# Optimization experiments

Measured on AMD Instinct MI355X. Metric: run time of the kernel, lower is better.

Reference implementation:

```python
import jax, jax.numpy as jnp
import numpy as np

N = 8192
E = 262144
IN_DIM, HID, OUT = 256, 256, 32


def setup_inputs() -> dict:
    key = jax.random.key(0)
    ks = jax.random.split(key, 10)
    features = jax.random.normal(ks[0], (N, IN_DIM), jnp.float32)
    noise = jax.random.normal(ks[1], (N, OUT), jnp.float32)
    src = jax.random.randint(ks[2], (E,), 0, N, jnp.int32)
    dst = jax.random.randint(ks[3], (E,), 0, N, jnp.int32)
    s = lambda fi, fo: 1.0 / np.sqrt(fi)
    W1 = jax.random.normal(ks[4], (IN_DIM, HID), jnp.float32) * s(IN_DIM, HID)
    W2 = jax.random.normal(ks[5], (HID, HID), jnp.float32) * s(HID, HID)
    W3 = jax.random.normal(ks[6], (HID, OUT), jnp.float32) * s(HID, OUT)
    b1 = jnp.zeros((HID,), jnp.float32)
    b2 = jnp.zeros((HID,), jnp.float32)
    b3 = jnp.zeros((OUT,), jnp.float32)
    fc_w = jax.random.normal(ks[7], (IN_DIM, OUT), jnp.float32) * s(IN_DIM, OUT)
    return dict(features=features, noise=noise, src=src, dst=dst,
                W1=W1, b1=b1, W2=W2, b2=b2, W3=W3, b3=b3, fc_w=fc_w)


def _degree_norms(src, dst, n):
    ones = jnp.ones_like(src, jnp.float32)
    out_deg = jax.ops.segment_sum(ones, src, num_segments=n)
    in_deg = jax.ops.segment_sum(ones, dst, num_segments=n)
    # DGL GraphConv norm='both' clamps degrees to min 1 before pow(-0.5)
    norm_src = jnp.maximum(out_deg, 1.0) ** -0.5  # [N]
    norm_dst = jnp.maximum(in_deg, 1.0) ** -0.5   # [N]
    return norm_src, norm_dst


def _graph_conv(x, src, dst, norm_src, norm_dst, W, b, n):
    # h = D_in^{-1/2} A D_out^{-1/2} x W + b, then relu
    h = x @ W                                  # transform first (smaller agg dim)
    m = (h * norm_src[:, None])[src]           # [E, F] gather + scale
    agg = jax.ops.segment_sum(m, dst, num_segments=n)
    return jax.nn.relu(agg * norm_dst[:, None] + b)


def reference(features, noise, src, dst, W1, b1, W2, b2, W3, b3, fc_w):
    n = features.shape[0]
    norm_s, norm_d = _degree_norms(src, dst, n)
    h = _graph_conv(features, src, dst, norm_s, norm_d, W1, b1, n)
    mean = _graph_conv(h, src, dst, norm_s, norm_d, W2, b2, n)
    log_std = _graph_conv(h, src, dst, norm_s, norm_d, W3, b3, n)
    # note: mean [N,HID] broadcasts against noise*exp(log_std) [N,OUT] only if
    # HID==OUT dims align; original code has mean from layer[1] (hidden_dim) and
    # log_std from layer[2] (out_dim). To keep the math runnable we follow the
    # VGAE intent: layer[1] and layer[2] both map to out_dim here (W2 below is
    # hidden->hidden, W3 hidden->out; mean uses W3-shaped branch). See notes.
    z = mean[:, :noise.shape[1]] if mean.shape[1] != noise.shape[1] else mean
    z = z + noise * jnp.exp(log_std)
    adj_rec = jax.nn.sigmoid(z @ z.T)          # [N, N] dense decoder
    seq_fts = features @ fc_w                  # Linear(in_dim, out_dim, bias=False)
    return adj_rec, z, seq_fts
```

## Files before the change

kernel.cpp:

```cpp
#include <hip/hip_runtime.h>
#include <hip/hip_fp16.h>

#define NNODES 8192
#define NEDGES 262144
#define NNOUT 67108864L

typedef _Float16 half8 __attribute__((ext_vector_type(8)));
typedef _Float16 half4 __attribute__((ext_vector_type(4)));
typedef float float4v __attribute__((ext_vector_type(4)));


__global__ __launch_bounds__(256) void prep_kernel(const float* __restrict__ W1, const float* __restrict__ W2,
                                                   const float* __restrict__ W3, const float* __restrict__ b2,
                                                   const float* __restrict__ b3, _Float16* __restrict__ W1th,
                                                   _Float16* __restrict__ W1tl, _Float16* __restrict__ Wzth,
                                                   _Float16* __restrict__ Wztl, float* __restrict__ bz,
                                                   int* __restrict__ degs) {
  int b = blockIdx.x, t = threadIdx.x;
  float w = W1[b * 256 + t];
  _Float16 wh = (_Float16)w;
  W1th[t * 256 + b] = wh;
  W1tl[t * 256 + b] = (_Float16)(w - (float)wh);
  if (b >= 64 && b < 128) {
    int c = b - 64;
    float v = (c < 32) ? W2[t * 256 + c] : W3[t * 32 + (c - 32)];
    _Float16 vh = (_Float16)v;
    Wzth[c * 256 + t] = vh;
    Wztl[c * 256 + t] = (_Float16)(v - (float)vh);
  }
  if (b == 128 && t < 64) bz[t] = (t < 32) ? b2[t] : b3[t - 32];
  if (b >= 192) degs[(b - 192) * 256 + t] = 0;
}

__global__ __launch_bounds__(256) void deg_kernel(const int* __restrict__ src, const int* __restrict__ dst,
                                                  int* __restrict__ out_deg, int* __restrict__ in_deg) {
  int e = blockIdx.x * 256 + threadIdx.x;
  if (e < NEDGES) {
    atomicAdd(&out_deg[src[e]], 1);
    atomicAdd(&in_deg[dst[e]], 1);
  }
}

__global__ __launch_bounds__(256) void scan_norm_kernel(const int* __restrict__ in_deg,
                                                        const int* __restrict__ out_deg,
                                                        int* __restrict__ row_ptr, int* __restrict__ cursor,
                                                        float* __restrict__ norm_src, float* __restrict__ norm_dst) {
  __shared__ int partial[256];
  int t = threadIdx.x;
  int base = t * 32;
  int local[32];
  int s = 0;
#pragma unroll
  for (int i = 0; i < 32; ++i) { local[i] = in_deg[base + i]; s += local[i]; }
  partial[t] = s;
  __syncthreads();
  for (int off = 1; off < 256; off <<= 1) {
    int v = (t >= off) ? partial[t - off] : 0;
    __syncthreads();
    partial[t] += v;
    __syncthreads();
  }
  int run = (t == 0) ? 0 : partial[t - 1];
  if (t == 0) row_ptr[0] = 0;
#pragma unroll
  for (int i = 0; i < 32; ++i) {
    int od = out_deg[base + i]; if (od < 1) od = 1;
    int id = local[i]; if (id < 1) id = 1;
    norm_src[base + i] = rsqrtf((float)od);
    norm_dst[base + i] = rsqrtf((float)id);
    cursor[base + i] = run;
    run += local[i];
    row_ptr[base + i + 1] = run;
  }
}

__global__ __launch_bounds__(256) void scatter_convert(const int* __restrict__ src, const int* __restrict__ dst,
                                                       int* __restrict__ cursor, int* __restrict__ csr,
                                                       const float* __restrict__ x, const float* __restrict__ norm_src,
                                                       _Float16* __restrict__ xs) {
  int b = blockIdx.x, t = threadIdx.x;
  if (b < 1024) {
    int e = b * 256 + t;
    int d = dst[e];
    int pos = atomicAdd(&cursor[d], 1);
    csr[pos] = src[e];
  }
  int i = b * 256 + t;
  int base = i * 4;
  float ns = norm_src[base >> 8];
  float4 v = *(const float4*)(x + base);
  half4 o = {(_Float16)(v.x * ns), (_Float16)(v.y * ns), (_Float16)(v.z * ns), (_Float16)(v.w * ns)};
  *(half4*)(xs + base) = o;
}


__global__ __launch_bounds__(256) void propagate_hl(const _Float16* __restrict__ xs, _Float16* __restrict__ Qh,
                                                    _Float16* __restrict__ Ql, const int* __restrict__ row_ptr,
                                                    const int* __restrict__ csr, const float* __restrict__ norm_dst) {
  int v = blockIdx.x * 4 + (threadIdx.x >> 6);
  int lane = threadIdx.x & 63;
  int beg = row_ptr[v], end = row_ptr[v + 1];
  float a0 = 0.f, a1 = 0.f, a2 = 0.f, a3 = 0.f;
  const _Float16* base = xs + 4 * lane;
  int e = beg;
  for (; e + 4 <= end; e += 4) {
    int s0 = csr[e], s1 = csr[e + 1], s2 = csr[e + 2], s3 = csr[e + 3];
    half4 v0 = *(const half4*)(base + (long)s0 * 256);
    half4 v1 = *(const half4*)(base + (long)s1 * 256);
    half4 v2 = *(const half4*)(base + (long)s2 * 256);
    half4 v3 = *(const half4*)(base + (long)s3 * 256);
    a0 += (float)v0.x + (float)v1.x + (float)v2.x + (float)v3.x;
    a1 += (float)v0.y + (float)v1.y + (float)v2.y + (float)v3.y;
    a2 += (float)v0.z + (float)v1.z + (float)v2.z + (float)v3.z;
    a3 += (float)v0.w + (float)v1.w + (float)v2.w + (float)v3.w;
  }
  for (; e < end; ++e) {
    half4 v0 = *(const half4*)(base + (long)csr[e] * 256);
    a0 += (float)v0.x; a1 += (float)v0.y; a2 += (float)v0.z; a3 += (float)v0.w;
  }
  float nd = norm_dst[v];
  a0 *= nd; a1 *= nd; a2 *= nd; a3 *= nd;
  _Float16 h0 = (_Float16)a0, h1 = (_Float16)a1, h2 = (_Float16)a2, h3 = (_Float16)a3;
  half4 qh = {h0, h1, h2, h3};
  half4 ql = {(_Float16)(a0 - (float)h0), (_Float16)(a1 - (float)h1),
              (_Float16)(a2 - (float)h2), (_Float16)(a3 - (float)h3)};
  *(half4*)(Qh + (long)v * 256 + 4 * lane) = qh;
  *(half4*)(Ql + (long)v * 256 + 4 * lane) = ql;
}


__global__ __launch_bounds__(256) void gemm1_mfma(const _Float16* __restrict__ Qh, const _Float16* __restrict__ Ql,
                                                  const _Float16* __restrict__ W1th, const _Float16* __restrict__ W1tl,
                                                  const float* __restrict__ b1, const float* __restrict__ norm_src,
                                                  _Float16* __restrict__ xs) {
  int tid = threadIdx.x;
  int wave = tid >> 6, lane = tid & 63;
  int l15 = lane & 15, lk = (lane >> 4) * 8;
  long rowBase = blockIdx.x * 64 + wave * 16;
  int colBase = blockIdx.y * 128;
  float4v acc[8] = {};
  for (int ks = 0; ks < 8; ++ks) {
    int k0 = ks * 32;
    half8 ah = *(const half8*)(Qh + (rowBase + l15) * 256 + k0 + lk);
    half8 al = *(const half8*)(Ql + (rowBase + l15) * 256 + k0 + lk);
#pragma unroll
    for (int ct = 0; ct < 8; ++ct) {
      long bo = (long)(colBase + ct * 16 + l15) * 256 + k0 + lk;
      half8 bh = *(const half8*)(W1th + bo);
      half8 bl = *(const half8*)(W1tl + bo);
      acc[ct] = __builtin_amdgcn_mfma_f32_16x16x32_f16(al, bh, acc[ct], 0, 0, 0);
      acc[ct] = __builtin_amdgcn_mfma_f32_16x16x32_f16(ah, bl, acc[ct], 0, 0, 0);
      acc[ct] = __builtin_amdgcn_mfma_f32_16x16x32_f16(ah, bh, acc[ct], 0, 0, 0);
    }
  }
  int crow = (lane >> 4) * 4;
#pragma unroll
  for (int ct = 0; ct < 8; ++ct) {
    int c = colBase + ct * 16 + l15;
    float bb = b1[c];
#pragma unroll
    for (int r = 0; r < 4; ++r) {
      long row = rowBase + crow + r;
      float v = fmaxf(acc[ct][r] + bb, 0.f) * norm_src[row];
      xs[row * 256 + c] = (_Float16)v;
    }
  }
}


__global__ __launch_bounds__(256) void gemmz_mfma(const _Float16* __restrict__ Qh, const _Float16* __restrict__ Ql,
                                                  const _Float16* __restrict__ Wzth, const _Float16* __restrict__ Wztl,
                                                  const float* __restrict__ bz, const float* __restrict__ noise,
                                                  float* __restrict__ zout, _Float16* __restrict__ Zh,
                                                  _Float16* __restrict__ Zl) {
  int tid = threadIdx.x;
  int wave = tid >> 6, lane = tid & 63;
  int l15 = lane & 15, lk = (lane >> 4) * 8;
  long rowBase = blockIdx.x * 64 + wave * 16;
  float4v acc[4] = {};
  for (int ks = 0; ks < 8; ++ks) {
    int k0 = ks * 32;
    half8 ah = *(const half8*)(Qh + (rowBase + l15) * 256 + k0 + lk);
    half8 al = *(const half8*)(Ql + (rowBase + l15) * 256 + k0 + lk);
#pragma unroll
    for (int ct = 0; ct < 4; ++ct) {
      long bo = (long)(ct * 16 + l15) * 256 + k0 + lk;
      half8 bh = *(const half8*)(Wzth + bo);
      half8 bl = *(const half8*)(Wztl + bo);
      acc[ct] = __builtin_amdgcn_mfma_f32_16x16x32_f16(al, bh, acc[ct], 0, 0, 0);
      acc[ct] = __builtin_amdgcn_mfma_f32_16x16x32_f16(ah, bl, acc[ct], 0, 0, 0);
      acc[ct] = __builtin_amdgcn_mfma_f32_16x16x32_f16(ah, bh, acc[ct], 0, 0, 0);
    }
  }
  int crow = (lane >> 4) * 4;
  float bm0 = bz[l15], bm1 = bz[16 + l15], bs0 = bz[32 + l15], bs1 = bz[48 + l15];
#pragma unroll
  for (int r = 0; r < 4; ++r) {
    long row = rowBase + crow + r;
    float me0 = fmaxf(acc[0][r] + bm0, 0.f);
    float me1 = fmaxf(acc[1][r] + bm1, 0.f);
    float ls0 = fmaxf(acc[2][r] + bs0, 0.f);
    float ls1 = fmaxf(acc[3][r] + bs1, 0.f);
    float n0 = noise[row * 32 + l15];
    float n1 = noise[row * 32 + 16 + l15];
    float z0 = me0 + n0 * __expf(ls0);
    float z1 = me1 + n1 * __expf(ls1);
    zout[row * 32 + l15] = z0;
    zout[row * 32 + 16 + l15] = z1;
    _Float16 h0 = (_Float16)z0, h1 = (_Float16)z1;
    Zh[row * 32 + l15] = h0;
    Zl[row * 32 + l15] = (_Float16)(z0 - (float)h0);
    Zh[row * 32 + 16 + l15] = h1;
    Zl[row * 32 + 16 + l15] = (_Float16)(z1 - (float)h1);
  }
}


__global__ __launch_bounds__(256) void adj_seq(const _Float16* __restrict__ Zh, const _Float16* __restrict__ Zl,
                                               float* __restrict__ out, const float* __restrict__ F,
                                               const float* __restrict__ Wf, float* __restrict__ seq) {
  int tid = threadIdx.x;
  if (blockIdx.x >= 64) {
    int sb = (blockIdx.x - 64) * 64 + blockIdx.y;
    int t = sb * 256 + tid;
    int row = t >> 3;
    int cq = (t & 7) * 4;
    float a0 = 0.f, a1 = 0.f, a2 = 0.f, a3 = 0.f;
    const float* frow = F + row * 256;
    for (int k = 0; k < 256; k += 4) {
      float4 fv = *(const float4*)(frow + k);
      float4 w0 = *(const float4*)(Wf + k * 32 + cq);
      float4 w1 = *(const float4*)(Wf + (k + 1) * 32 + cq);
      float4 w2 = *(const float4*)(Wf + (k + 2) * 32 + cq);
      float4 w3 = *(const float4*)(Wf + (k + 3) * 32 + cq);
      a0 = fmaf(fv.x, w0.x, fmaf(fv.y, w1.x, fmaf(fv.z, w2.x, fmaf(fv.w, w3.x, a0))));
      a1 = fmaf(fv.x, w0.y, fmaf(fv.y, w1.y, fmaf(fv.z, w2.y, fmaf(fv.w, w3.y, a1))));
      a2 = fmaf(fv.x, w0.z, fmaf(fv.y, w1.z, fmaf(fv.z, w2.z, fmaf(fv.w, w3.z, a2))));
      a3 = fmaf(fv.x, w0.w, fmaf(fv.y, w1.w, fmaf(fv.z, w2.w, fmaf(fv.w, w3.w, a3))));
    }
    float4 o = {a0, a1, a2, a3};
    *(float4*)&seq[row * 32 + cq] = o;
    return;
  }
  int wave = tid >> 6;
  int lane = tid & 63;
  long rowBase = (long)blockIdx.y * 128 + wave * 32;
  long colBase = (long)blockIdx.x * 128;
  int l15 = lane & 15;
  int lk = (lane >> 4) * 8;
  half8 ah0 = *(const half8*)(Zh + (rowBase + l15) * 32 + lk);
  half8 al0 = *(const half8*)(Zl + (rowBase + l15) * 32 + lk);
  half8 ah1 = *(const half8*)(Zh + (rowBase + 16 + l15) * 32 + lk);
  half8 al1 = *(const half8*)(Zl + (rowBase + 16 + l15) * 32 + lk);
  int crow = (lane >> 4) * 4;
#pragma unroll
  for (int ct = 0; ct < 8; ++ct) {
    half8 bh = *(const half8*)(Zh + (colBase + ct * 16 + l15) * 32 + lk);
    half8 bl = *(const half8*)(Zl + (colBase + ct * 16 + l15) * 32 + lk);
    float4v acc0 = {}, acc1 = {};
    acc0 = __builtin_amdgcn_mfma_f32_16x16x32_f16(al0, bh, acc0, 0, 0, 0);
    acc0 = __builtin_amdgcn_mfma_f32_16x16x32_f16(ah0, bl, acc0, 0, 0, 0);
    acc0 = __builtin_amdgcn_mfma_f32_16x16x32_f16(ah0, bh, acc0, 0, 0, 0);
    acc1 = __builtin_amdgcn_mfma_f32_16x16x32_f16(al1, bh, acc1, 0, 0, 0);
    acc1 = __builtin_amdgcn_mfma_f32_16x16x32_f16(ah1, bl, acc1, 0, 0, 0);
    acc1 = __builtin_amdgcn_mfma_f32_16x16x32_f16(ah1, bh, acc1, 0, 0, 0);
    long c = colBase + ct * 16 + l15;
#pragma unroll
    for (int r = 0; r < 4; ++r) {
      float s0 = __builtin_amdgcn_rcpf(1.f + __expf(-acc0[r]));
      float s1 = __builtin_amdgcn_rcpf(1.f + __expf(-acc1[r]));
      __builtin_nontemporal_store(s0, &out[(rowBase + crow + r) * 8192 + c]);
      __builtin_nontemporal_store(s1, &out[(rowBase + 16 + crow + r) * 8192 + c]);
    }
  }
}


extern "C" void kernel_launch(void* const* d_in, const int* in_sizes, int n_in,
                              void* d_out, int out_size, void* d_ws, size_t ws_size,
                              hipStream_t stream) {
  const float* features = (const float*)d_in[0];
  const float* noise    = (const float*)d_in[1];
  const int*   src      = (const int*)d_in[2];
  const int*   dst      = (const int*)d_in[3];
  const float* W1       = (const float*)d_in[4];
  const float* b1       = (const float*)d_in[5];
  const float* W2       = (const float*)d_in[6];
  const float* b2       = (const float*)d_in[7];
  const float* W3       = (const float*)d_in[8];
  const float* b3       = (const float*)d_in[9];
  const float* fcw      = (const float*)d_in[10];

  float* out = (float*)d_out;

  int* ws_i    = (int*)d_ws;
  int* out_deg = ws_i;
  int* in_deg  = ws_i + 8192;
  int* row_ptr = ws_i + 16384;
  int* cursor  = ws_i + 24832;
  int* csr     = ws_i + 33024;
  float* norm_src = (float*)(ws_i + 295168);
  float* norm_dst = (float*)(ws_i + 303360);
  _Float16* Zh = (_Float16*)(ws_i + 311552);
  _Float16* Zl = (_Float16*)(ws_i + 442624);

  float* adj      = out;
  float* zbuf     = out + NNOUT;
  float* seq      = out + NNOUT + 262144;
  _Float16* xs    = (_Float16*)out;
  _Float16* Qh    = (_Float16*)(out + 1048576);
  _Float16* Ql    = (_Float16*)(out + 2097152);
  _Float16* W1th  = (_Float16*)(out + 3145728);
  _Float16* W1tl  = (_Float16*)(out + 3178496);
  _Float16* Wzth  = (_Float16*)(out + 3211264);
  _Float16* Wztl  = (_Float16*)(out + 3219456);
  float*    bz    = out + 3227648;

  prep_kernel<<<256, 256, 0, stream>>>(W1, W2, W3, b2, b3, W1th, W1tl, Wzth, Wztl, bz, out_deg);
  deg_kernel<<<NEDGES / 256, 256, 0, stream>>>(src, dst, out_deg, in_deg);
  scan_norm_kernel<<<1, 256, 0, stream>>>(in_deg, out_deg, row_ptr, cursor, norm_src, norm_dst);
  scatter_convert<<<2048, 256, 0, stream>>>(src, dst, cursor, csr, features, norm_src, xs);

  propagate_hl<<<2048, 256, 0, stream>>>(xs, Qh, Ql, row_ptr, csr, norm_dst);
  gemm1_mfma<<<dim3(128, 2), 256, 0, stream>>>(Qh, Ql, W1th, W1tl, b1, norm_src, xs);

  propagate_hl<<<2048, 256, 0, stream>>>(xs, Qh, Ql, row_ptr, csr, norm_dst);
  gemmz_mfma<<<128, 256, 0, stream>>>(Qh, Ql, Wzth, Wztl, bz, noise, zbuf, Zh, Zl);

  adj_seq<<<dim3(68, 64), 256, 0, stream>>>(Zh, Zl, adj, features, fcw, seq);
}
```

Measured before the change: 220.9 us.

## Stage adjacency tiles through LDS for coalesced stores; move seq GEMM into scatter

The dense decoder now writes its sigmoid tile into a per-wave LDS slab and stores rows back as float4 vectors, replacing scattered scalar nontemporal stores with coalesced wide writes. The features@fc_w projection moves out of the adjacency kernel and into the scatter/convert kernel as extra blocks, so the adjacency launch is uniform. The cost is LDS usage and two block-wide barriers per half tile, which may limit occupancy. It also drops the nontemporal hint on the 256MB output stream.

```diff
diff --git a/kernel.cpp b/kernel.cpp
--- a/kernel.cpp
+++ b/kernel.cpp
@@ -74,11 +74,34 @@
   }
 }
 
-__global__ __launch_bounds__(256) void scatter_convert(const int* __restrict__ src, const int* __restrict__ dst,
-                                                       int* __restrict__ cursor, int* __restrict__ csr,
-                                                       const float* __restrict__ x, const float* __restrict__ norm_src,
-                                                       _Float16* __restrict__ xs) {
+__global__ __launch_bounds__(256) void scatter_convert_seq(const int* __restrict__ src, const int* __restrict__ dst,
+                                                           int* __restrict__ cursor, int* __restrict__ csr,
+                                                           const float* __restrict__ x,
+                                                           const float* __restrict__ norm_src,
+                                                           _Float16* __restrict__ xs, const float* __restrict__ Wf,
+                                                           float* __restrict__ seq) {
   int b = blockIdx.x, t = threadIdx.x;
+  if (b >= 2048) {
+    int tt = (b - 2048) * 256 + t;
+    int row = tt >> 3;
+    int cq = (tt & 7) * 4;
+    float a0 = 0.f, a1 = 0.f, a2 = 0.f, a3 = 0.f;
+    const float* frow = x + row * 256;
+    for (int k = 0; k < 256; k += 4) {
+      float4 fv = *(const float4*)(frow + k);
+      float4 w0 = *(const float4*)(Wf + k * 32 + cq);
+      float4 w1 = *(const float4*)(Wf + (k + 1) * 32 + cq);
+      float4 w2 = *(const float4*)(Wf + (k + 2) * 32 + cq);
+      float4 w3 = *(const float4*)(Wf + (k + 3) * 32 + cq);
+      a0 = fmaf(fv.x, w0.x, fmaf(fv.y, w1.x, fmaf(fv.z, w2.x, fmaf(fv.w, w3.x, a0))));
+      a1 = fmaf(fv.x, w0.y, fmaf(fv.y, w1.y, fmaf(fv.z, w2.y, fmaf(fv.w, w3.y, a1))));
+      a2 = fmaf(fv.x, w0.z, fmaf(fv.y, w1.z, fmaf(fv.z, w2.z, fmaf(fv.w, w3.z, a2))));
+      a3 = fmaf(fv.x, w0.w, fmaf(fv.y, w1.w, fmaf(fv.z, w2.w, fmaf(fv.w, w3.w, a3))));
+    }
+    float4 o = {a0, a1, a2, a3};
+    *(float4*)&seq[row * 32 + cq] = o;
+    return;
+  }
   if (b < 1024) {
     int e = b * 256 + t;
     int d = dst[e];
@@ -216,32 +239,10 @@
 }
 
 
-__global__ __launch_bounds__(256) void adj_seq(const _Float16* __restrict__ Zh, const _Float16* __restrict__ Zl,
-                                               float* __restrict__ out, const float* __restrict__ F,
-                                               const float* __restrict__ Wf, float* __restrict__ seq) {
+__global__ __launch_bounds__(256) void adj_mfma(const _Float16* __restrict__ Zh, const _Float16* __restrict__ Zl,
+                                                float* __restrict__ out) {
+  __shared__ __align__(16) float lds[4][32][68];
   int tid = threadIdx.x;
-  if (blockIdx.x >= 64) {
-    int sb = (blockIdx.x - 64) * 64 + blockIdx.y;
-    int t = sb * 256 + tid;
-    int row = t >> 3;
-    int cq = (t & 7) * 4;
-    float a0 = 0.f, a1 = 0.f, a2 = 0.f, a3 = 0.f;
-    const float* frow = F + row * 256;
-    for (int k = 0; k < 256; k += 4) {
-      float4 fv = *(const float4*)(frow + k);
-      float4 w0 = *(const float4*)(Wf + k * 32 + cq);
-      float4 w1 = *(const float4*)(Wf + (k + 1) * 32 + cq);
-      float4 w2 = *(const float4*)(Wf + (k + 2) * 32 + cq);
-      float4 w3 = *(const float4*)(Wf + (k + 3) * 32 + cq);
-      a0 = fmaf(fv.x, w0.x, fmaf(fv.y, w1.x, fmaf(fv.z, w2.x, fmaf(fv.w, w3.x, a0))));
-      a1 = fmaf(fv.x, w0.y, fmaf(fv.y, w1.y, fmaf(fv.z, w2.y, fmaf(fv.w, w3.y, a1))));
-      a2 = fmaf(fv.x, w0.z, fmaf(fv.y, w1.z, fmaf(fv.z, w2.z, fmaf(fv.w, w3.z, a2))));
-      a3 = fmaf(fv.x, w0.w, fmaf(fv.y, w1.w, fmaf(fv.z, w2.w, fmaf(fv.w, w3.w, a3))));
-    }
-    float4 o = {a0, a1, a2, a3};
-    *(float4*)&seq[row * 32 + cq] = o;
-    return;
-  }
   int wave = tid >> 6;
   int lane = tid & 63;
   long rowBase = (long)blockIdx.y * 128 + wave * 32;
@@ -253,25 +254,35 @@
   half8 ah1 = *(const half8*)(Zh + (rowBase + 16 + l15) * 32 + lk);
   half8 al1 = *(const half8*)(Zl + (rowBase + 16 + l15) * 32 + lk);
   int crow = (lane >> 4) * 4;
-#pragma unroll
-  for (int ct = 0; ct < 8; ++ct) {
-    half8 bh = *(const half8*)(Zh + (colBase + ct * 16 + l15) * 32 + lk);
-    half8 bl = *(const half8*)(Zl + (colBase + ct * 16 + l15) * 32 + lk);
-    float4v acc0 = {}, acc1 = {};
-    acc0 = __builtin_amdgcn_mfma_f32_16x16x32_f16(al0, bh, acc0, 0, 0, 0);
-    acc0 = __builtin_amdgcn_mfma_f32_16x16x32_f16(ah0, bl, acc0, 0, 0, 0);
-    acc0 = __builtin_amdgcn_mfma_f32_16x16x32_f16(ah0, bh, acc0, 0, 0, 0);
-    acc1 = __builtin_amdgcn_mfma_f32_16x16x32_f16(al1, bh, acc1, 0, 0, 0);
-    acc1 = __builtin_amdgcn_mfma_f32_16x16x32_f16(ah1, bl, acc1, 0, 0, 0);
-    acc1 = __builtin_amdgcn_mfma_f32_16x16x32_f16(ah1, bh, acc1, 0, 0, 0);
-    long c = colBase + ct * 16 + l15;
-#pragma unroll
-    for (int r = 0; r < 4; ++r) {
-      float s0 = __builtin_amdgcn_rcpf(1.f + __expf(-acc0[r]));
-      float s1 = __builtin_amdgcn_rcpf(1.f + __expf(-acc1[r]));
-      __builtin_nontemporal_store(s0, &out[(rowBase + crow + r) * 8192 + c]);
-      __builtin_nontemporal_store(s1, &out[(rowBase + 16 + crow + r) * 8192 + c]);
-    }
+  float* slab = &lds[wave][0][0];
+#pragma unroll
+  for (int h = 0; h < 2; ++h) {
+#pragma unroll
+    for (int ct = 0; ct < 4; ++ct) {
+      int cg = h * 4 + ct;
+      half8 bh = *(const half8*)(Zh + (colBase + cg * 16 + l15) * 32 + lk);
+      half8 bl = *(const half8*)(Zl + (colBase + cg * 16 + l15) * 32 + lk);
+      float4v acc0 = {}, acc1 = {};
+      acc0 = __builtin_amdgcn_mfma_f32_16x16x32_f16(al0, bh, acc0, 0, 0, 0);
+      acc0 = __builtin_amdgcn_mfma_f32_16x16x32_f16(ah0, bl, acc0, 0, 0, 0);
+      acc0 = __builtin_amdgcn_mfma_f32_16x16x32_f16(ah0, bh, acc0, 0, 0, 0);
+      acc1 = __builtin_amdgcn_mfma_f32_16x16x32_f16(al1, bh, acc1, 0, 0, 0);
+      acc1 = __builtin_amdgcn_mfma_f32_16x16x32_f16(ah1, bl, acc1, 0, 0, 0);
+      acc1 = __builtin_amdgcn_mfma_f32_16x16x32_f16(ah1, bh, acc1, 0, 0, 0);
+#pragma unroll
+      for (int r = 0; r < 4; ++r) {
+        slab[(crow + r) * 68 + ct * 16 + l15] = __builtin_amdgcn_rcpf(1.f + __expf(-acc0[r]));
+        slab[(16 + crow + r) * 68 + ct * 16 + l15] = __builtin_amdgcn_rcpf(1.f + __expf(-acc1[r]));
+      }
+    }
+    __syncthreads();
+#pragma unroll
+    for (int i = 0; i < 8; ++i) {
+      int rr = 4 * i + (lane >> 4);
+      float4 v = *(const float4*)&slab[rr * 68 + 4 * l15];
+      *(float4*)&out[(rowBase + rr) * 8192 + colBase + h * 64 + 4 * l15] = v;
+    }
+    __syncthreads();
   }
 }
 
@@ -319,7 +330,7 @@
   prep_kernel<<<256, 256, 0, stream>>>(W1, W2, W3, b2, b3, W1th, W1tl, Wzth, Wztl, bz, out_deg);
   deg_kernel<<<NEDGES / 256, 256, 0, stream>>>(src, dst, out_deg, in_deg);
   scan_norm_kernel<<<1, 256, 0, stream>>>(in_deg, out_deg, row_ptr, cursor, norm_src, norm_dst);
-  scatter_convert<<<2048, 256, 0, stream>>>(src, dst, cursor, csr, features, norm_src, xs);
+  scatter_convert_seq<<<2304, 256, 0, stream>>>(src, dst, cursor, csr, features, norm_src, xs, fcw, seq);
 
   propagate_hl<<<2048, 256, 0, stream>>>(xs, Qh, Ql, row_ptr, csr, norm_dst);
   gemm1_mfma<<<dim3(128, 2), 256, 0, stream>>>(Qh, Ql, W1th, W1tl, b1, norm_src, xs);
@@ -327,5 +338,5 @@
   propagate_hl<<<2048, 256, 0, stream>>>(xs, Qh, Ql, row_ptr, csr, norm_dst);
   gemmz_mfma<<<128, 256, 0, stream>>>(Qh, Ql, Wzth, Wztl, bz, noise, zbuf, Zh, Zl);
 
-  adj_seq<<<dim3(68, 64), 256, 0, stream>>>(Zh, Zl, adj, features, fcw, seq);
-}
+  adj_mfma<<<dim3(64, 64), 256, 0, stream>>>(Zh, Zl, adj);
+}
```

After: 206.7 us. -6.4%, faster.
